# Kernel tuning notes

Hardware: AMD Instinct MI355X
Metric: run time of the kernel (lower is better)

Reference implementation:

```python
import jax, jax.numpy as jnp
import numpy as np

B, N, E, L, S = 8, 64, 256, 128, 2  # graphs, nodes, edges, latent dim, MPN steps


def setup_inputs() -> dict:
    key = jax.random.key(0)
    ks = jax.random.split(key, 16)

    def lin(k, fi, fo):
        return (jax.random.normal(k, (fi, fo), jnp.float32) / np.sqrt(fi).astype(np.float32))

    return {
        "x": jax.random.normal(ks[0], (B, N, L), jnp.float32),
        "edge_attr": jax.random.normal(ks[1], (B, E, L), jnp.float32),
        "u": jax.random.normal(ks[2], (B, L), jnp.float32),
        "spdist": jax.random.uniform(ks[3], (B, N, N), jnp.float32),
        "edge_index": jax.random.randint(ks[4], (B, 2, E), 0, N),
        # encoders
        "W_node_enc": lin(ks[5], 2 * L + 1, L), "b_node_enc": jnp.zeros(L, jnp.float32),
        "W_edge_enc": lin(ks[6], L, L), "b_edge_enc": jnp.zeros(L, jnp.float32),
        "W_glob_enc": lin(ks[7], L, L), "b_glob_enc": jnp.zeros(L, jnp.float32),
        # per-step edge / node update MLPs (stacked over S steps)
        "W_edge_upd": jnp.stack([lin(ks[8 + s], 4 * L, L) for s in range(S)]),
        "b_edge_upd": jnp.zeros((S, L), jnp.float32),
        "W_node_upd": jnp.stack([lin(ks[10 + s], 3 * L, L) for s in range(S)]),
        "b_node_upd": jnp.zeros((S, L), jnp.float32),
        # final edge scorer (per_dest_embedding_to_score)
        "W_score": lin(ks[12], L, 1), "b_score": jnp.zeros(1, jnp.float32),
    }


def reference(x, edge_attr, u, spdist, edge_index,
              W_node_enc, b_node_enc, W_edge_enc, b_edge_enc,
              W_glob_enc, b_glob_enc, W_edge_upd, b_edge_upd,
              W_node_upd, b_node_upd, W_score, b_score):
    act = jax.nn.leaky_relu  # torch LeakyReLU default slope 0.01
    n_steps = W_edge_upd.shape[0]

    def per_graph(xg, eg, ug, sdg, eig):
        Ng, Lg = xg.shape
        Eg = eg.shape[0]
        src, dst = eig[0], eig[1]
        # Augmented node features: graph copy d, node i -> [x_i, x_d, spdist[d, i]]
        # (matches x.repeat(N,1) / x.repeat_interleave(N,0) + chunk(N))
        x_tile = jnp.broadcast_to(xg[None, :, :], (Ng, Ng, Lg))
        x_dest = jnp.broadcast_to(xg[:, None, :], (Ng, Ng, Lg))
        xa = jnp.concatenate([x_tile, x_dest, sdg[..., None]], axis=-1)  # [Nd, N, 2L+1]
        h = act(xa @ W_node_enc + b_node_enc)                            # [Nd, N, L]
        ee = act(eg @ W_edge_enc + b_edge_enc)                           # [E, L]
        ee = jnp.broadcast_to(ee[None], (Ng, Eg, Lg))                    # [Nd, E, L]
        gg = act(ug @ W_glob_enc + b_glob_enc)                           # [L]
        for s in range(n_steps):
            gb_e = jnp.broadcast_to(gg, (Ng, Eg, Lg))
            ein = jnp.concatenate([ee, h[:, src], h[:, dst], gb_e], axis=-1)  # [Nd, E, 4L]
            ee = ee + act(ein @ W_edge_upd[s] + b_edge_upd[s])
            agg = jax.vmap(lambda ef: jax.ops.segment_sum(ef, dst, num_segments=Ng))(ee)  # [Nd, N, L]
            gb_n = jnp.broadcast_to(gg, (Ng, Ng, Lg))
            nin = jnp.concatenate([h, agg, gb_n], axis=-1)                    # [Nd, N, 3L]
            h = h + act(nin @ W_node_upd[s] + b_node_upd[s])
        scores = (ee @ W_score + b_score)[..., 0]  # [Nd, E]
        # reshape(N, -1).t().flatten() per graph -> [E * N]
        return scores.T.reshape(-1)

    out = jax.vmap(per_graph)(x, edge_attr, u, spdist, edge_index)  # [B, E*N]
    return out.reshape(-1)
```

## Files before the change

kernel.cpp:

```cpp
#include <hip/hip_runtime.h>
#include <hip/hip_bf16.h>


typedef __attribute__((ext_vector_type(8))) __bf16 bf16x8;
typedef __attribute__((ext_vector_type(4))) __bf16 bf16x4;
typedef __attribute__((ext_vector_type(4))) float  floatx4;

#define MFMA16(a, b, c) __builtin_amdgcn_mfma_f32_16x16x32_bf16((a), (b), (c), 0, 0, 0)

__device__ __forceinline__ float leaky(float x) { return x > 0.f ? x : 0.01f * x; }

#define WS_WT     0
#define WS_XAP    327680
#define WS_XDP    589824
#define WS_EE0    851968
#define WS_CE     1376256
#define WS_CN     1384448
#define WS_CSROFF 1392640
#define WS_CSREID 1394944

#define LDE 140

__global__ __launch_bounds__(256) void mpn_prep(
    const float* __restrict__ x,
    const float* __restrict__ ea,
    const float* __restrict__ u,
    const int*   __restrict__ eidx,
    const float* __restrict__ Wne,
    const float* __restrict__ bne,
    const float* __restrict__ Wee,
    const float* __restrict__ bee,
    const float* __restrict__ Wge,
    const float* __restrict__ bge,
    const float* __restrict__ Weu,
    const float* __restrict__ beu,
    const float* __restrict__ Wnu,
    const float* __restrict__ bnu,
    char* __restrict__ ws)
{
  __shared__ __align__(16) __bf16 smem[384 * LDE];

  const int b = blockIdx.x, tid = threadIdx.x;
  __bf16* wt  = (__bf16*)(ws + WS_WT);
  float*  xap = (float*)(ws + WS_XAP);
  float*  xdp = (float*)(ws + WS_XDP);
  __bf16* ee0 = (__bf16*)(ws + WS_EE0);
  float*  cev = (float*)(ws + WS_CE);
  float*  cnv = (float*)(ws + WS_CN);
  int* csroff = (int*)(ws + WS_CSROFF);
  int* csreid = (int*)(ws + WS_CSREID);

  if (b < 20) {
    const int m = b >> 1, half = b & 1;
    const int s = m / 5, t = m % 5;
    const float* src = (t < 3) ? (Weu + (size_t)(s*512 + t*128)*128)
                               : (Wnu + (size_t)(s*384 + (t-3)*128)*128);
    for (int it = 0; it < 4; ++it) {
      int p = it*256 + tid;
      int mq = half*4 + (p >> 8);
      int c  = (p >> 6) & 3;
      int l  = p & 63;
      int fr = mq*16 + (l & 15);
      int kb = c*32 + (l >> 4)*8;
      __bf16* dst = &wt[m*16384 + ((mq*4 + c)*64 + l)*8];
      #pragma unroll
      for (int j = 0; j < 8; ++j)
        dst[j] = (__bf16)src[(kb + j)*128 + fr];
    }
  } else if (b < 28) {
    const int g = b - 20;
    __shared__ float gg_sh[128];
    __shared__ int dst_sh[256];
    __shared__ int cnt_sh[64];
    __shared__ int off_sh[65];
    if (tid < 128) {
      float acc = bge[tid];
      for (int k = 0; k < 128; ++k)
        acc += u[g*128 + k] * Wge[k*128 + tid];
      gg_sh[tid] = leaky(acc);
    }
    dst_sh[tid] = eidx[g*512 + 256 + tid];
    __syncthreads();
    {
      const int s = tid >> 7, f = tid & 127;
      float ac = beu[s*128 + f];
      float an = bnu[s*128 + f];
      #pragma unroll 8
      for (int k = 0; k < 128; ++k) {
        float gk = gg_sh[k];
        ac += gk * Weu[(s*512 + 384 + k)*128 + f];
        an += gk * Wnu[(s*384 + 256 + k)*128 + f];
      }
      cev[(g*2 + s)*128 + f] = ac;
      cnv[(g*2 + s)*128 + f] = an;
    }
    if (tid < 64) {
      int c = 0;
      for (int e = 0; e < 256; ++e) c += (dst_sh[e] == tid) ? 1 : 0;
      cnt_sh[tid] = c;
    }
    __syncthreads();
    if (tid == 0) {
      int o = 0;
      for (int n = 0; n < 64; ++n) { off_sh[n] = o; o += cnt_sh[n]; }
      off_sh[64] = o;
    }
    __syncthreads();
    if (tid < 65) csroff[g*72 + tid] = off_sh[tid];
    if (tid < 64) {
      int o = off_sh[tid];
      for (int e = 0; e < 256; ++e)
        if (dst_sh[e] == tid) csreid[g*256 + (o++)] = e;
    }
  } else if (b < 36) {
    const int g = b - 28;
    __bf16* s_a = smem;
    __bf16* s_w = smem + 256*LDE;
    #pragma unroll
    for (int it = 0; it < 32; ++it) {
      int c = it*256 + tid;
      int row = c >> 5, f4 = (c & 31)*4;
      floatx4 v = *(const floatx4*)&ea[(size_t)(g*256 + row)*128 + f4];
      bf16x4 o;
      #pragma unroll
      for (int r = 0; r < 4; ++r) o[r] = (__bf16)v[r];
      *(bf16x4*)&s_a[row*LDE + f4] = o;
    }
    #pragma unroll 8
    for (int it = 0; it < 64; ++it) {
      int k = it*2 + (tid >> 7), f = tid & 127;
      s_w[f*LDE + k] = (__bf16)Wee[k*128 + f];
    }
    __syncthreads();
    const int w = tid >> 6, l = tid & 63, q = l >> 4, xn = l & 15;
    bf16x8 bea[4][4];
    #pragma unroll
    for (int t = 0; t < 4; ++t) {
      int e = w*64 + t*16 + xn;
      #pragma unroll
      for (int c = 0; c < 4; ++c)
        bea[t][c] = *(const bf16x8*)&s_a[e*LDE + c*32 + q*8];
    }
    #pragma unroll
    for (int m = 0; m < 8; ++m) {
      floatx4 acc[4];
      #pragma unroll
      for (int t = 0; t < 4; ++t) acc[t] = (floatx4)0.f;
      const int fr = m*16 + xn;
      #pragma unroll
      for (int c = 0; c < 4; ++c) {
        bf16x8 aw = *(const bf16x8*)&s_w[fr*LDE + c*32 + q*8];
        #pragma unroll
        for (int t = 0; t < 4; ++t) acc[t] = MFMA16(aw, bea[t][c], acc[t]);
      }
      const int f0 = m*16 + q*4;
      floatx4 b4 = *(const floatx4*)&bee[f0];
      #pragma unroll
      for (int t = 0; t < 4; ++t) {
        int e = w*64 + t*16 + xn;
        bf16x4 o;
        #pragma unroll
        for (int r = 0; r < 4; ++r) o[r] = (__bf16)leaky(acc[t][r] + b4[r]);
        *(bf16x4*)&ee0[(size_t)(g*256 + e)*128 + f0] = o;
      }
    }
  } else {
    const int g = b - 36;
    __bf16* s_x  = smem;
    __bf16* s_wa = smem + 64*LDE;
    __bf16* s_wb = smem + 192*LDE;
    #pragma unroll
    for (int it = 0; it < 8; ++it) {
      int c = it*256 + tid;
      int row = c >> 5, f4 = (c & 31)*4;
      floatx4 v = *(const floatx4*)&x[(size_t)(g*64 + row)*128 + f4];
      bf16x4 o;
      #pragma unroll
      for (int r = 0; r < 4; ++r) o[r] = (__bf16)v[r];
      *(bf16x4*)&s_x[row*LDE + f4] = o;
    }
    #pragma unroll 8
    for (int it = 0; it < 64; ++it) {
      int k = it*2 + (tid >> 7), f = tid & 127;
      s_wa[f*LDE + k] = (__bf16)Wne[k*128 + f];
      s_wb[f*LDE + k] = (__bf16)Wne[(128 + k)*128 + f];
    }
    __syncthreads();
    const int w = tid >> 6, l = tid & 63, q = l >> 4, xn = l & 15;
    const int i = w*16 + xn;
    bf16x8 bx[4];
    #pragma unroll
    for (int c = 0; c < 4; ++c)
      bx[c] = *(const bf16x8*)&s_x[i*LDE + c*32 + q*8];
    #pragma unroll
    for (int m = 0; m < 8; ++m) {
      floatx4 aa = (floatx4)0.f, ab = (floatx4)0.f;
      const int fr = m*16 + xn;
      #pragma unroll
      for (int c = 0; c < 4; ++c) {
        bf16x8 aw = *(const bf16x8*)&s_wa[fr*LDE + c*32 + q*8];
        aa = MFMA16(aw, bx[c], aa);
      }
      #pragma unroll
      for (int c = 0; c < 4; ++c) {
        bf16x8 aw = *(const bf16x8*)&s_wb[fr*LDE + c*32 + q*8];
        ab = MFMA16(aw, bx[c], ab);
      }
      const int f0 = m*16 + q*4;
      floatx4 bn4 = *(const floatx4*)&bne[f0];
      floatx4 oa;
      #pragma unroll
      for (int r = 0; r < 4; ++r) oa[r] = aa[r] + bn4[r];
      *(floatx4*)&xap[(size_t)(g*64 + i)*128 + f0] = oa;
      *(floatx4*)&xdp[(size_t)(g*64 + i)*128 + f0] = ab;
    }
  }
}

__global__ __launch_bounds__(512, 2) void mpn_main(
    const float* __restrict__ spdist,
    const int*   __restrict__ eidx,
    const float* __restrict__ Wne,
    const float* __restrict__ wscore,
    const float* __restrict__ bscore,
    const char* __restrict__ ws,
    float* __restrict__ out)
{
  __shared__ __align__(16) __bf16 s_ee[256*LDE];
  __shared__ __align__(16) __bf16 s_h [64*LDE];
  __shared__ __align__(16) __bf16 s_p2[64*LDE];
  __shared__ __align__(16) __bf16 s_p3[64*LDE];
  __shared__ int s_off[65];
  __shared__ int s_eid[256];
  __shared__ float s_sc[256];

  const __bf16* wt  = (const __bf16*)(ws + WS_WT);
  const float*  xap = (const float*)(ws + WS_XAP);
  const float*  xdp = (const float*)(ws + WS_XDP);
  const __bf16* ee0 = (const __bf16*)(ws + WS_EE0);
  const float*  cev = (const float*)(ws + WS_CE);
  const float*  cnv = (const float*)(ws + WS_CN);
  const int* csroff = (const int*)(ws + WS_CSROFF);
  const int* csreid = (const int*)(ws + WS_CSREID);

  const int tid = threadIdx.x;
  const int w = tid >> 6, l = tid & 63;
  const int q = l >> 4, xn = l & 15;
  const int wp = w >> 1, mh = w & 1;
  const int lane8 = l*8;
  const int fme = w*16 + q*4;
  const int g = blockIdx.x >> 6, d = blockIdx.x & 63;

  if (tid < 65) s_off[tid] = csroff[g*72 + tid];
  if (tid < 256) s_eid[tid] = csreid[g*256 + tid];

  {
    const int f = tid & 127, ib = tid >> 7;
    float xdpv = xdp[(g*64 + d)*128 + f];
    float wspv = Wne[256*128 + f];
    #pragma unroll
    for (int j = 0; j < 16; ++j) {
      int i = ib + 4*j;
      float sp = spdist[(g*64 + d)*64 + i];
      float v = xap[(g*64 + i)*128 + f] + xdpv + sp*wspv;
      s_h[i*LDE + f] = (__bf16)leaky(v);
    }
  }
  #pragma unroll
  for (int it = 0; it < 8; ++it) {
    int c = it*512 + tid;
    int row = c >> 4, col = c & 15;
    *(bf16x8*)&s_ee[row*LDE + col*8] = *(const bf16x8*)&ee0[(g*256 + row)*128 + col*8];
  }

  int mySrc[4], myDst[4];
  #pragma unroll
  for (int t = 0; t < 4; ++t) {
    int e = wp*64 + t*16 + xn;
    mySrc[t] = eidx[g*512 + e];
    myDst[t] = eidx[g*512 + 256 + e];
  }
  __syncthreads();

  for (int s = 0; s < 2; ++s) {
    const __bf16* W1T = wt + (s*5 + 0)*16384;
    const __bf16* W2T = wt + (s*5 + 1)*16384;
    const __bf16* W3T = wt + (s*5 + 2)*16384;
    const __bf16* N1T = wt + (s*5 + 3)*16384;
    const __bf16* N2T = wt + (s*5 + 4)*16384;

    bf16x8 w2f[4], w3f[4], n1f[4], n2f[4], w1f[4][4];
    #pragma unroll
    for (int c = 0; c < 4; ++c) {
      w2f[c] = *(const bf16x8*)&W2T[(w*4 + c)*512 + lane8];
      w3f[c] = *(const bf16x8*)&W3T[(w*4 + c)*512 + lane8];
    }
    #pragma unroll
    for (int mm = 0; mm < 4; ++mm)
      #pragma unroll
      for (int c = 0; c < 4; ++c)
        w1f[mm][c] = *(const bf16x8*)&W1T[((mh*4 + mm)*4 + c)*512 + lane8];
    if (s == 0) {
      #pragma unroll
      for (int c = 0; c < 4; ++c) {
        n1f[c] = *(const bf16x8*)&N1T[(w*4 + c)*512 + lane8];
        n2f[c] = *(const bf16x8*)&N2T[(w*4 + c)*512 + lane8];
      }
    }

    {
      floatx4 ce4 = *(const floatx4*)&cev[(g*2 + s)*128 + fme];
      #pragma unroll
      for (int t = 0; t < 4; ++t) {
        const int i = t*16 + xn;
        floatx4 a2 = (floatx4)0.f, a3 = (floatx4)0.f;
        #pragma unroll
        for (int c = 0; c < 4; ++c) {
          bf16x8 bh = *(const bf16x8*)&s_h[i*LDE + c*32 + q*8];
          a2 = MFMA16(w2f[c], bh, a2);
          a3 = MFMA16(w3f[c], bh, a3);
        }
        bf16x4 o2, o3;
        #pragma unroll
        for (int r = 0; r < 4; ++r) { o2[r] = (__bf16)a2[r]; o3[r] = (__bf16)(a3[r] + ce4[r]); }
        *(bf16x4*)&s_p2[i*LDE + fme] = o2;
        *(bf16x4*)&s_p3[i*LDE + fme] = o3;
      }
    }
    floatx4 acc[4][4];
    {
      bf16x8 be[4][4];
      #pragma unroll
      for (int t = 0; t < 4; ++t) {
        int e = wp*64 + t*16 + xn;
        #pragma unroll
        for (int c = 0; c < 4; ++c)
          be[t][c] = *(const bf16x8*)&s_ee[e*LDE + c*32 + q*8];
      }
      #pragma unroll
      for (int mm = 0; mm < 4; ++mm) {
        #pragma unroll
        for (int t = 0; t < 4; ++t) acc[mm][t] = (floatx4)0.f;
        #pragma unroll
        for (int c = 0; c < 4; ++c) {
          #pragma unroll
          for (int t = 0; t < 4; ++t) acc[mm][t] = MFMA16(w1f[mm][c], be[t][c], acc[mm][t]);
        }
      }
    }
    __syncthreads();

    {
      #pragma unroll
      for (int mm = 0; mm < 4; ++mm) {
        const int m = mh*4 + mm;
        const int f0 = m*16 + q*4;
        #pragma unroll
        for (int t = 0; t < 4; ++t) {
          int e = wp*64 + t*16 + xn;
          bf16x4 old = *(const bf16x4*)&s_ee[e*LDE + f0];
          bf16x4 v2  = *(const bf16x4*)&s_p2[mySrc[t]*LDE + f0];
          bf16x4 v3  = *(const bf16x4*)&s_p3[myDst[t]*LDE + f0];
          bf16x4 res;
          #pragma unroll
          for (int r = 0; r < 4; ++r) {
            float vv = acc[mm][t][r] + (float)v2[r] + (float)v3[r];
            res[r] = (__bf16)((float)old[r] + leaky(vv));
          }
          *(bf16x4*)&s_ee[e*LDE + f0] = res;
        }
      }
    }
    __syncthreads();

    if (s == 0) {
      floatx4 a4[4];
      {
        const int node = tid >> 3;
        const int fs = (tid & 7)*16;
        float av[16];
        #pragma unroll
        for (int j = 0; j < 16; ++j) av[j] = 0.f;
        const int b0 = s_off[node], b1 = s_off[node + 1];
        for (int idx = b0; idx < b1; ++idx) {
          int e = s_eid[idx];
          #pragma unroll
          for (int cc = 0; cc < 2; ++cc) {
            bf16x8 vv = *(const bf16x8*)&s_ee[e*LDE + fs + cc*8];
            #pragma unroll
            for (int j = 0; j < 8; ++j) av[cc*8 + j] += (float)vv[j];
          }
        }
        #pragma unroll
        for (int cc = 0; cc < 2; ++cc) {
          bf16x8 o;
          #pragma unroll
          for (int j = 0; j < 8; ++j) o[j] = (__bf16)av[cc*8 + j];
          *(bf16x8*)&s_p2[node*LDE + fs + cc*8] = o;
        }
        #pragma unroll
        for (int t = 0; t < 4; ++t) {
          const int i = t*16 + xn;
          floatx4 a = (floatx4)0.f;
          #pragma unroll
          for (int c = 0; c < 4; ++c) {
            bf16x8 bh = *(const bf16x8*)&s_h[i*LDE + c*32 + q*8];
            a = MFMA16(n1f[c], bh, a);
          }
          a4[t] = a;
        }
      }
      __syncthreads();

      {
        floatx4 cn4 = *(const floatx4*)&cnv[(g*2 + s)*128 + fme];
        #pragma unroll
        for (int t = 0; t < 4; ++t) {
          const int i = t*16 + xn;
          floatx4 a = a4[t];
          #pragma unroll
          for (int c = 0; c < 4; ++c) {
            bf16x8 bg = *(const bf16x8*)&s_p2[i*LDE + c*32 + q*8];
            a = MFMA16(n2f[c], bg, a);
          }
          bf16x4 old = *(const bf16x4*)&s_h[i*LDE + fme];
          bf16x4 res;
          #pragma unroll
          for (int r = 0; r < 4; ++r)
            res[r] = (__bf16)((float)old[r] + leaky(a[r] + cn4[r]));
          *(bf16x4*)&s_h[i*LDE + fme] = res;
        }
      }
      __syncthreads();
    }
  }

  {
    const int e = tid & 255, hh = tid >> 8;
    float acc = 0.f;
    #pragma unroll
    for (int c = 0; c < 8; ++c) {
      bf16x8 vv = *(const bf16x8*)&s_ee[e*LDE + hh*64 + c*8];
      #pragma unroll
      for (int j = 0; j < 8; ++j) acc += (float)vv[j] * wscore[hh*64 + c*8 + j];
    }
    if (hh == 1) s_sc[e] = acc;
    __syncthreads();
    if (hh == 0) out[g*16384 + e*64 + d] = acc + s_sc[e] + bscore[0];
  }
}

extern "C" void kernel_launch(void* const* d_in, const int* in_sizes, int n_in,
                              void* d_out, int out_size, void* d_ws, size_t ws_size,
                              hipStream_t stream) {
  (void)in_sizes; (void)n_in; (void)out_size; (void)ws_size;
  const float* x   = (const float*)d_in[0];
  const float* ea  = (const float*)d_in[1];
  const float* u   = (const float*)d_in[2];
  const float* sp  = (const float*)d_in[3];
  const int*   ei  = (const int*)d_in[4];
  const float* Wne = (const float*)d_in[5];
  const float* bne = (const float*)d_in[6];
  const float* Wee = (const float*)d_in[7];
  const float* bee = (const float*)d_in[8];
  const float* Wge = (const float*)d_in[9];
  const float* bge = (const float*)d_in[10];
  const float* Weu = (const float*)d_in[11];
  const float* beu = (const float*)d_in[12];
  const float* Wnu = (const float*)d_in[13];
  const float* bnu = (const float*)d_in[14];
  const float* Wsc = (const float*)d_in[15];
  const float* bsc = (const float*)d_in[16];
  char* ws = (char*)d_ws;

  hipLaunchKernelGGL(mpn_prep, dim3(44), dim3(256), 0, stream,
                     x, ea, u, ei, Wne, bne, Wee, bee, Wge, bge, Weu, beu, Wnu, bnu, ws);
  hipLaunchKernelGGL(mpn_main, dim3(512), dim3(512), 0, stream,
                     sp, ei, Wne, Wsc, bsc, (const char*)ws, (float*)d_out);
}
```

Baseline: 155.4 us.

## Fuse prep and main kernels into one cooperative launch with grid sync

Merges the preprocessing kernel and the main message-passing kernel into a single cooperative kernel, with a grid-wide sync separating the prep phase from the per-destination computation. The grid shrinks from 512 to 256 blocks, so each block now handles two destination copies in sequence, reloading h and ee each time. This removes one kernel launch and the gap between the two kernels. In exchange it adds a grid barrier, halves the block-level parallelism, and runs the prep phase on only 44 blocks using half their threads.

Result: slower. 323.2 us (+107.9%).

```diff
diff --git a/kernel.cpp b/kernel.cpp
--- a/kernel.cpp
+++ b/kernel.cpp
@@ -1,6 +1,9 @@
 #include <hip/hip_runtime.h>
 #include <hip/hip_bf16.h>
-
+#include <hip/hip_cooperative_groups.h>
+
+
+namespace cg = cooperative_groups;
 
 typedef __attribute__((ext_vector_type(8))) __bf16 bf16x8;
 typedef __attribute__((ext_vector_type(4))) __bf16 bf16x4;
@@ -21,10 +24,11 @@
 
 #define LDE 140
 
-__global__ __launch_bounds__(256) void mpn_prep(
+__global__ __launch_bounds__(512, 2) void mpn_fused(
     const float* __restrict__ x,
     const float* __restrict__ ea,
     const float* __restrict__ u,
+    const float* __restrict__ spdist,
     const int*   __restrict__ eidx,
     const float* __restrict__ Wne,
     const float* __restrict__ bne,
@@ -36,52 +40,67 @@
     const float* __restrict__ beu,
     const float* __restrict__ Wnu,
     const float* __restrict__ bnu,
-    char* __restrict__ ws)
+    const float* __restrict__ wscore,
+    const float* __restrict__ bscore,
+    char* __restrict__ ws,
+    float* __restrict__ out)
 {
-  __shared__ __align__(16) __bf16 smem[384 * LDE];
-
-  const int b = blockIdx.x, tid = threadIdx.x;
-  __bf16* wt  = (__bf16*)(ws + WS_WT);
-  float*  xap = (float*)(ws + WS_XAP);
-  float*  xdp = (float*)(ws + WS_XDP);
-  __bf16* ee0 = (__bf16*)(ws + WS_EE0);
-  float*  cev = (float*)(ws + WS_CE);
-  float*  cnv = (float*)(ws + WS_CN);
-  int* csroff = (int*)(ws + WS_CSROFF);
-  int* csreid = (int*)(ws + WS_CSREID);
-
-  if (b < 20) {
-    const int m = b >> 1, half = b & 1;
-    const int s = m / 5, t = m % 5;
-    const float* src = (t < 3) ? (Weu + (size_t)(s*512 + t*128)*128)
-                               : (Wnu + (size_t)(s*384 + (t-3)*128)*128);
-    for (int it = 0; it < 4; ++it) {
-      int p = it*256 + tid;
-      int mq = half*4 + (p >> 8);
-      int c  = (p >> 6) & 3;
-      int l  = p & 63;
-      int fr = mq*16 + (l & 15);
-      int kb = c*32 + (l >> 4)*8;
-      __bf16* dst = &wt[m*16384 + ((mq*4 + c)*64 + l)*8];
-      #pragma unroll
-      for (int j = 0; j < 8; ++j)
-        dst[j] = (__bf16)src[(kb + j)*128 + fr];
-    }
-  } else if (b < 28) {
-    const int g = b - 20;
-    __shared__ float gg_sh[128];
-    __shared__ int dst_sh[256];
-    __shared__ int cnt_sh[64];
-    __shared__ int off_sh[65];
+  __shared__ __align__(16) __bf16 pool[448 * LDE];
+  __shared__ int s_off[65];
+  __shared__ int s_eid[256];
+  __shared__ float s_sc[256];
+
+  __bf16* s_ee = pool;
+  __bf16* s_h  = pool + 256*LDE;
+  __bf16* s_p2 = pool + 320*LDE;
+  __bf16* s_p3 = pool + 384*LDE;
+
+  __bf16* wt   = (__bf16*)(ws + WS_WT);
+  float*  xap  = (float*)(ws + WS_XAP);
+  float*  xdp  = (float*)(ws + WS_XDP);
+  __bf16* ee0  = (__bf16*)(ws + WS_EE0);
+  float*  cev  = (float*)(ws + WS_CE);
+  float*  cnv  = (float*)(ws + WS_CN);
+  int* csroff  = (int*)(ws + WS_CSROFF);
+  int* csreid  = (int*)(ws + WS_CSREID);
+
+  const int bid = blockIdx.x, tid = threadIdx.x;
+
+  if (bid < 20) {
+    if (tid < 256) {
+      const int m = bid >> 1, half = bid & 1;
+      const int s = m / 5, t = m % 5;
+      const float* src = (t < 3) ? (Weu + (size_t)(s*512 + t*128)*128)
+                                 : (Wnu + (size_t)(s*384 + (t-3)*128)*128);
+      for (int it = 0; it < 4; ++it) {
+        int p = it*256 + tid;
+        int mq = half*4 + (p >> 8);
+        int c  = (p >> 6) & 3;
+        int l  = p & 63;
+        int fr = mq*16 + (l & 15);
+        int kb = c*32 + (l >> 4)*8;
+        __bf16* dst = &wt[m*16384 + ((mq*4 + c)*64 + l)*8];
+        #pragma unroll
+        for (int j = 0; j < 8; ++j)
+          dst[j] = (__bf16)src[(kb + j)*128 + fr];
+      }
+    }
+  } else if (bid < 28) {
+    const int g = bid - 20;
+    char* pb = (char*)pool;
+    float* gg_sh = (float*)pb;
+    int* dst_sh  = (int*)(pb + 512);
+    int* cnt_sh  = (int*)(pb + 1536);
+    int* off_sh  = (int*)(pb + 1792);
     if (tid < 128) {
       float acc = bge[tid];
       for (int k = 0; k < 128; ++k)
         acc += u[g*128 + k] * Wge[k*128 + tid];
       gg_sh[tid] = leaky(acc);
     }
-    dst_sh[tid] = eidx[g*512 + 256 + tid];
-    __syncthreads();
-    {
+    if (tid < 256) dst_sh[tid] = eidx[g*512 + 256 + tid];
+    __syncthreads();
+    if (tid < 256) {
       const int s = tid >> 7, f = tid & 127;
       float ac = beu[s*128 + f];
       float an = bnu[s*128 + f];
@@ -112,166 +131,130 @@
       for (int e = 0; e < 256; ++e)
         if (dst_sh[e] == tid) csreid[g*256 + (o++)] = e;
     }
-  } else if (b < 36) {
-    const int g = b - 28;
-    __bf16* s_a = smem;
-    __bf16* s_w = smem + 256*LDE;
-    #pragma unroll
-    for (int it = 0; it < 32; ++it) {
-      int c = it*256 + tid;
-      int row = c >> 5, f4 = (c & 31)*4;
-      floatx4 v = *(const floatx4*)&ea[(size_t)(g*256 + row)*128 + f4];
-      bf16x4 o;
-      #pragma unroll
-      for (int r = 0; r < 4; ++r) o[r] = (__bf16)v[r];
-      *(bf16x4*)&s_a[row*LDE + f4] = o;
-    }
-    #pragma unroll 8
-    for (int it = 0; it < 64; ++it) {
-      int k = it*2 + (tid >> 7), f = tid & 127;
-      s_w[f*LDE + k] = (__bf16)Wee[k*128 + f];
-    }
-    __syncthreads();
-    const int w = tid >> 6, l = tid & 63, q = l >> 4, xn = l & 15;
-    bf16x8 bea[4][4];
-    #pragma unroll
-    for (int t = 0; t < 4; ++t) {
-      int e = w*64 + t*16 + xn;
-      #pragma unroll
-      for (int c = 0; c < 4; ++c)
-        bea[t][c] = *(const bf16x8*)&s_a[e*LDE + c*32 + q*8];
-    }
-    #pragma unroll
-    for (int m = 0; m < 8; ++m) {
-      floatx4 acc[4];
-      #pragma unroll
-      for (int t = 0; t < 4; ++t) acc[t] = (floatx4)0.f;
-      const int fr = m*16 + xn;
-      #pragma unroll
-      for (int c = 0; c < 4; ++c) {
-        bf16x8 aw = *(const bf16x8*)&s_w[fr*LDE + c*32 + q*8];
-        #pragma unroll
-        for (int t = 0; t < 4; ++t) acc[t] = MFMA16(aw, bea[t][c], acc[t]);
-      }
-      const int f0 = m*16 + q*4;
-      floatx4 b4 = *(const floatx4*)&bee[f0];
+  } else if (bid < 36) {
+    const int g = bid - 28;
+    __bf16* s_a = pool;
+    __bf16* s_w = pool + 256*LDE;
+    if (tid < 256) {
+      #pragma unroll
+      for (int it = 0; it < 32; ++it) {
+        int c = it*256 + tid;
+        int row = c >> 5, f4 = (c & 31)*4;
+        floatx4 v = *(const floatx4*)&ea[(size_t)(g*256 + row)*128 + f4];
+        bf16x4 o;
+        #pragma unroll
+        for (int r = 0; r < 4; ++r) o[r] = (__bf16)v[r];
+        *(bf16x4*)&s_a[row*LDE + f4] = o;
+      }
+      #pragma unroll 8
+      for (int it = 0; it < 64; ++it) {
+        int k = it*2 + (tid >> 7), f = tid & 127;
+        s_w[f*LDE + k] = (__bf16)Wee[k*128 + f];
+      }
+    }
+    __syncthreads();
+    if (tid < 256) {
+      const int w = tid >> 6, l = tid & 63, q = l >> 4, xn = l & 15;
+      bf16x8 bea[4][4];
       #pragma unroll
       for (int t = 0; t < 4; ++t) {
         int e = w*64 + t*16 + xn;
+        #pragma unroll
+        for (int c = 0; c < 4; ++c)
+          bea[t][c] = *(const bf16x8*)&s_a[e*LDE + c*32 + q*8];
+      }
+      #pragma unroll
+      for (int m = 0; m < 8; ++m) {
+        floatx4 acc[4];
+        #pragma unroll
+        for (int t = 0; t < 4; ++t) acc[t] = (floatx4)0.f;
+        const int fr = m*16 + xn;
+        #pragma unroll
+        for (int c = 0; c < 4; ++c) {
+          bf16x8 aw = *(const bf16x8*)&s_w[fr*LDE + c*32 + q*8];
+          #pragma unroll
+          for (int t = 0; t < 4; ++t) acc[t] = MFMA16(aw, bea[t][c], acc[t]);
+        }
+        const int f0 = m*16 + q*4;
+        floatx4 b4 = *(const floatx4*)&bee[f0];
+        #pragma unroll
+        for (int t = 0; t < 4; ++t) {
+          int e = w*64 + t*16 + xn;
+          bf16x4 o;
+          #pragma unroll
+          for (int r = 0; r < 4; ++r) o[r] = (__bf16)leaky(acc[t][r] + b4[r]);
+          *(bf16x4*)&ee0[(size_t)(g*256 + e)*128 + f0] = o;
+        }
+      }
+    }
+  } else if (bid < 44) {
+    const int g = bid - 36;
+    __bf16* s_x  = pool;
+    __bf16* s_wa = pool + 64*LDE;
+    __bf16* s_wb = pool + 192*LDE;
+    if (tid < 256) {
+      #pragma unroll
+      for (int it = 0; it < 8; ++it) {
+        int c = it*256 + tid;
+        int row = c >> 5, f4 = (c & 31)*4;
+        floatx4 v = *(const floatx4*)&x[(size_t)(g*64 + row)*128 + f4];
         bf16x4 o;
         #pragma unroll
-        for (int r = 0; r < 4; ++r) o[r] = (__bf16)leaky(acc[t][r] + b4[r]);
-        *(bf16x4*)&ee0[(size_t)(g*256 + e)*128 + f0] = o;
-      }
-    }
-  } else {
-    const int g = b - 36;
-    __bf16* s_x  = smem;
-    __bf16* s_wa = smem + 64*LDE;
-    __bf16* s_wb = smem + 192*LDE;
-    #pragma unroll
-    for (int it = 0; it < 8; ++it) {
-      int c = it*256 + tid;
-      int row = c >> 5, f4 = (c & 31)*4;
-      floatx4 v = *(const floatx4*)&x[(size_t)(g*64 + row)*128 + f4];
-      bf16x4 o;
-      #pragma unroll
-      for (int r = 0; r < 4; ++r) o[r] = (__bf16)v[r];
-      *(bf16x4*)&s_x[row*LDE + f4] = o;
-    }
-    #pragma unroll 8
-    for (int it = 0; it < 64; ++it) {
-      int k = it*2 + (tid >> 7), f = tid & 127;
-      s_wa[f*LDE + k] = (__bf16)Wne[k*128 + f];
-      s_wb[f*LDE + k] = (__bf16)Wne[(128 + k)*128 + f];
-    }
-    __syncthreads();
-    const int w = tid >> 6, l = tid & 63, q = l >> 4, xn = l & 15;
-    const int i = w*16 + xn;
-    bf16x8 bx[4];
-    #pragma unroll
-    for (int c = 0; c < 4; ++c)
-      bx[c] = *(const bf16x8*)&s_x[i*LDE + c*32 + q*8];
-    #pragma unroll
-    for (int m = 0; m < 8; ++m) {
-      floatx4 aa = (floatx4)0.f, ab = (floatx4)0.f;
-      const int fr = m*16 + xn;
-      #pragma unroll
-      for (int c = 0; c < 4; ++c) {
-        bf16x8 aw = *(const bf16x8*)&s_wa[fr*LDE + c*32 + q*8];
-        aa = MFMA16(aw, bx[c], aa);
-      }
-      #pragma unroll
-      for (int c = 0; c < 4; ++c) {
-        bf16x8 aw = *(const bf16x8*)&s_wb[fr*LDE + c*32 + q*8];
-        ab = MFMA16(aw, bx[c], ab);
-      }
-      const int f0 = m*16 + q*4;
-      floatx4 bn4 = *(const floatx4*)&bne[f0];
-      floatx4 oa;
-      #pragma unroll
-      for (int r = 0; r < 4; ++r) oa[r] = aa[r] + bn4[r];
-      *(floatx4*)&xap[(size_t)(g*64 + i)*128 + f0] = oa;
-      *(floatx4*)&xdp[(size_t)(g*64 + i)*128 + f0] = ab;
+        for (int r = 0; r < 4; ++r) o[r] = (__bf16)v[r];
+        *(bf16x4*)&s_x[row*LDE + f4] = o;
+      }
+      #pragma unroll 8
+      for (int it = 0; it < 64; ++it) {
+        int k = it*2 + (tid >> 7), f = tid & 127;
+        s_wa[f*LDE + k] = (__bf16)Wne[k*128 + f];
+        s_wb[f*LDE + k] = (__bf16)Wne[(128 + k)*128 + f];
+      }
+    }
+    __syncthreads();
+    if (tid < 256) {
+      const int w = tid >> 6, l = tid & 63, q = l >> 4, xn = l & 15;
+      const int i = w*16 + xn;
+      bf16x8 bx[4];
+      #pragma unroll
+      for (int c = 0; c < 4; ++c)
+        bx[c] = *(const bf16x8*)&s_x[i*LDE + c*32 + q*8];
+      #pragma unroll
+      for (int m = 0; m < 8; ++m) {
+        floatx4 aa = (floatx4)0.f, ab = (floatx4)0.f;
+        const int fr = m*16 + xn;
+        #pragma unroll
+        for (int c = 0; c < 4; ++c) {
+          bf16x8 aw = *(const bf16x8*)&s_wa[fr*LDE + c*32 + q*8];
+          aa = MFMA16(aw, bx[c], aa);
+        }
+        #pragma unroll
+        for (int c = 0; c < 4; ++c) {
+          bf16x8 aw = *(const bf16x8*)&s_wb[fr*LDE + c*32 + q*8];
+          ab = MFMA16(aw, bx[c], ab);
+        }
+        const int f0 = m*16 + q*4;
+        floatx4 bn4 = *(const floatx4*)&bne[f0];
+        floatx4 oa;
+        #pragma unroll
+        for (int r = 0; r < 4; ++r) oa[r] = aa[r] + bn4[r];
+        *(floatx4*)&xap[(size_t)(g*64 + i)*128 + f0] = oa;
+        *(floatx4*)&xdp[(size_t)(g*64 + i)*128 + f0] = ab;
+      }
     }
   }
-}
-
-__global__ __launch_bounds__(512, 2) void mpn_main(
-    const float* __restrict__ spdist,
-    const int*   __restrict__ eidx,
-    const float* __restrict__ Wne,
-    const float* __restrict__ wscore,
-    const float* __restrict__ bscore,
-    const char* __restrict__ ws,
-    float* __restrict__ out)
-{
-  __shared__ __align__(16) __bf16 s_ee[256*LDE];
-  __shared__ __align__(16) __bf16 s_h [64*LDE];
-  __shared__ __align__(16) __bf16 s_p2[64*LDE];
-  __shared__ __align__(16) __bf16 s_p3[64*LDE];
-  __shared__ int s_off[65];
-  __shared__ int s_eid[256];
-  __shared__ float s_sc[256];
-
-  const __bf16* wt  = (const __bf16*)(ws + WS_WT);
-  const float*  xap = (const float*)(ws + WS_XAP);
-  const float*  xdp = (const float*)(ws + WS_XDP);
-  const __bf16* ee0 = (const __bf16*)(ws + WS_EE0);
-  const float*  cev = (const float*)(ws + WS_CE);
-  const float*  cnv = (const float*)(ws + WS_CN);
-  const int* csroff = (const int*)(ws + WS_CSROFF);
-  const int* csreid = (const int*)(ws + WS_CSREID);
-
-  const int tid = threadIdx.x;
+
+  __threadfence();
+  cg::this_grid().sync();
+
   const int w = tid >> 6, l = tid & 63;
   const int q = l >> 4, xn = l & 15;
   const int wp = w >> 1, mh = w & 1;
   const int lane8 = l*8;
   const int fme = w*16 + q*4;
-  const int g = blockIdx.x >> 6, d = blockIdx.x & 63;
+  const int g = bid >> 5, dp = bid & 31;
 
   if (tid < 65) s_off[tid] = csroff[g*72 + tid];
   if (tid < 256) s_eid[tid] = csreid[g*256 + tid];
-
-  {
-    const int f = tid & 127, ib = tid >> 7;
-    float xdpv = xdp[(g*64 + d)*128 + f];
-    float wspv = Wne[256*128 + f];
-    #pragma unroll
-    for (int j = 0; j < 16; ++j) {
-      int i = ib + 4*j;
-      float sp = spdist[(g*64 + d)*64 + i];
-      float v = xap[(g*64 + i)*128 + f] + xdpv + sp*wspv;
-      s_h[i*LDE + f] = (__bf16)leaky(v);
-    }
-  }
-  #pragma unroll
-  for (int it = 0; it < 8; ++it) {
-    int c = it*512 + tid;
-    int row = c >> 4, col = c & 15;
-    *(bf16x8*)&s_ee[row*LDE + col*8] = *(const bf16x8*)&ee0[(g*256 + row)*128 + col*8];
-  }
 
   int mySrc[4], myDst[4];
   #pragma unroll
@@ -280,173 +263,196 @@
     mySrc[t] = eidx[g*512 + e];
     myDst[t] = eidx[g*512 + 256 + e];
   }
-  __syncthreads();
-
-  for (int s = 0; s < 2; ++s) {
-    const __bf16* W1T = wt + (s*5 + 0)*16384;
-    const __bf16* W2T = wt + (s*5 + 1)*16384;
-    const __bf16* W3T = wt + (s*5 + 2)*16384;
-    const __bf16* N1T = wt + (s*5 + 3)*16384;
-    const __bf16* N2T = wt + (s*5 + 4)*16384;
-
-    bf16x8 w2f[4], w3f[4], n1f[4], n2f[4], w1f[4][4];
+
+  for (int r = 0; r < 2; ++r) {
+    const int d = dp*2 + r;
+
+    {
+      const int f = tid & 127, ib = tid >> 7;
+      float xdpv = xdp[(g*64 + d)*128 + f];
+      float wspv = Wne[256*128 + f];
+      #pragma unroll
+      for (int j = 0; j < 16; ++j) {
+        int i = ib + 4*j;
+        float sp = spdist[(g*64 + d)*64 + i];
+        float v = xap[(g*64 + i)*128 + f] + xdpv + sp*wspv;
+        s_h[i*LDE + f] = (__bf16)leaky(v);
+      }
+    }
     #pragma unroll
-    for (int c = 0; c < 4; ++c) {
-      w2f[c] = *(const bf16x8*)&W2T[(w*4 + c)*512 + lane8];
-      w3f[c] = *(const bf16x8*)&W3T[(w*4 + c)*512 + lane8];
-    }
-    #pragma unroll
-    for (int mm = 0; mm < 4; ++mm)
-      #pragma unroll
-      for (int c = 0; c < 4; ++c)
-        w1f[mm][c] = *(const bf16x8*)&W1T[((mh*4 + mm)*4 + c)*512 + lane8];
-    if (s == 0) {
+    for (int it = 0; it < 8; ++it) {
+      int c = it*512 + tid;
+      int row = c >> 4, col = c & 15;
+      *(bf16x8*)&s_ee[row*LDE + col*8] = *(const bf16x8*)&ee0[(g*256 + row)*128 + col*8];
+    }
+    __syncthreads();
+
+    for (int s = 0; s < 2; ++s) {
+      const __bf16* W1T = wt + (s*5 + 0)*16384;
+      const __bf16* W2T = wt + (s*5 + 1)*16384;
+      const __bf16* W3T = wt + (s*5 + 2)*16384;
+      const __bf16* N1T = wt + (s*5 + 3)*16384;
+      const __bf16* N2T = wt + (s*5 + 4)*16384;
+
+      bf16x8 w2f[4], w3f[4], n1f[4], n2f[4], w1f[4][4];
       #pragma unroll
       for (int c = 0; c < 4; ++c) {
-        n1f[c] = *(const bf16x8*)&N1T[(w*4 + c)*512 + lane8];
-        n2f[c] = *(const bf16x8*)&N2T[(w*4 + c)*512 + lane8];
-      }
-    }
-
-    {
-      floatx4 ce4 = *(const floatx4*)&cev[(g*2 + s)*128 + fme];
-      #pragma unroll
-      for (int t = 0; t < 4; ++t) {
-        const int i = t*16 + xn;
-        floatx4 a2 = (floatx4)0.f, a3 = (floatx4)0.f;
+        w2f[c] = *(const bf16x8*)&W2T[(w*4 + c)*512 + lane8];
+        w3f[c] = *(const bf16x8*)&W3T[(w*4 + c)*512 + lane8];
+      }
+      #pragma unroll
+      for (int mm = 0; mm < 4; ++mm)
+        #pragma unroll
+        for (int c = 0; c < 4; ++c)
+          w1f[mm][c] = *(const bf16x8*)&W1T[((mh*4 + mm)*4 + c)*512 + lane8];
+      if (s == 0) {
         #pragma unroll
         for (int c = 0; c < 4; ++c) {
-          bf16x8 bh = *(const bf16x8*)&s_h[i*LDE + c*32 + q*8];
-          a2 = MFMA16(w2f[c], bh, a2);
-          a3 = MFMA16(w3f[c], bh, a3);
-        }
-        bf16x4 o2, o3;
-        #pragma unroll
-        for (int r = 0; r < 4; ++r) { o2[r] = (__bf16)a2[r]; o3[r] = (__bf16)(a3[r] + ce4[r]); }
-        *(bf16x4*)&s_p2[i*LDE + fme] = o2;
-        *(bf16x4*)&s_p3[i*LDE + fme] = o3;
-      }
-    }
-    floatx4 acc[4][4];
-    {
-      bf16x8 be[4][4];
-      #pragma unroll
-      for (int t = 0; t < 4; ++t) {
-        int e = wp*64 + t*16 + xn;
-        #pragma unroll
-        for (int c = 0; c < 4; ++c)
-          be[t][c] = *(const bf16x8*)&s_ee[e*LDE + c*32 + q*8];
-      }
-      #pragma unroll
-      for (int mm = 0; mm < 4; ++mm) {
-        #pragma unroll
-        for (int t = 0; t < 4; ++t) acc[mm][t] = (floatx4)0.f;
-        #pragma unroll
-        for (int c = 0; c < 4; ++c) {
-          #pragma unroll
-          for (int t = 0; t < 4; ++t) acc[mm][t] = MFMA16(w1f[mm][c], be[t][c], acc[mm][t]);
-        }
-      }
-    }
-    __syncthreads();
-
-    {
-      #pragma unroll
-      for (int mm = 0; mm < 4; ++mm) {
-        const int m = mh*4 + mm;
-        const int f0 = m*16 + q*4;
+          n1f[c] = *(const bf16x8*)&N1T[(w*4 + c)*512 + lane8];
+          n2f[c] = *(const bf16x8*)&N2T[(w*4 + c)*512 + lane8];
+        }
+      }
+
+      {
+        floatx4 ce4 = *(const floatx4*)&cev[(g*2 + s)*128 + fme];
+        #pragma unroll
+        for (int t = 0; t < 4; ++t) {
+          const int i = t*16 + xn;
+          floatx4 a2 = (floatx4)0.f, a3 = (floatx4)0.f;
+          #pragma unroll
+          for (int c = 0; c < 4; ++c) {
+            bf16x8 bh = *(const bf16x8*)&s_h[i*LDE + c*32 + q*8];
+            a2 = MFMA16(w2f[c], bh, a2);
+            a3 = MFMA16(w3f[c], bh, a3);
+          }
+          bf16x4 o2, o3;
+          #pragma unroll
+          for (int r2 = 0; r2 < 4; ++r2) { o2[r2] = (__bf16)a2[r2]; o3[r2] = (__bf16)(a3[r2] + ce4[r2]); }
+          *(bf16x4*)&s_p2[i*LDE + fme] = o2;
+          *(bf16x4*)&s_p3[i*LDE + fme] = o3;
+        }
+      }
+      floatx4 acc[4][4];
+      {
+        bf16x8 be[4][4];
         #pragma unroll
         for (int t = 0; t < 4; ++t) {
           int e = wp*64 + t*16 + xn;
-          bf16x4 old = *(const bf16x4*)&s_ee[e*LDE + f0];
-          bf16x4 v2  = *(const bf16x4*)&s_p2[mySrc[t]*LDE + f0];
-          bf16x4 v3  = *(const bf16x4*)&s_p3[myDst[t]*LDE + f0];
-          bf16x4 res;
-          #pragma unroll
-          for (int r = 0; r < 4; ++r) {
-            float vv = acc[mm][t][r] + (float)v2[r] + (float)v3[r];
-            res[r] = (__bf16)((float)old[r] + leaky(vv));
-          }
-          *(bf16x4*)&s_ee[e*LDE + f0] = res;
-        }
-      }
-    }
-    __syncthreads();
-
-    if (s == 0) {
-      floatx4 a4[4];
+          #pragma unroll
+          for (int c = 0; c < 4; ++c)
+            be[t][c] = *(const bf16x8*)&s_ee[e*LDE + c*32 + q*8];
+        }
+        #pragma unroll
+        for (int mm = 0; mm < 4; ++mm) {
+          #pragma unroll
+          for (int t = 0; t < 4; ++t) acc[mm][t] = (floatx4)0.f;
+          #pragma unroll
+          for (int c = 0; c < 4; ++c) {
+            #pragma unroll
+            for (int t = 0; t < 4; ++t) acc[mm][t] = MFMA16(w1f[mm][c], be[t][c], acc[mm][t]);
+          }
+        }
+      }
+      __syncthreads();
+
       {
-        const int node = tid >> 3;
-        const int fs = (tid & 7)*16;
-        float av[16];
-        #pragma unroll
-        for (int j = 0; j < 16; ++j) av[j] = 0.f;
-        const int b0 = s_off[node], b1 = s_off[node + 1];
-        for (int idx = b0; idx < b1; ++idx) {
-          int e = s_eid[idx];
+        #pragma unroll
+        for (int mm = 0; mm < 4; ++mm) {
+          const int m = mh*4 + mm;
+          const int f0 = m*16 + q*4;
+          #pragma unroll
+          for (int t = 0; t < 4; ++t) {
+            int e = wp*64 + t*16 + xn;
+            bf16x4 old = *(const bf16x4*)&s_ee[e*LDE + f0];
+            bf16x4 v2  = *(const bf16x4*)&s_p2[mySrc[t]*LDE + f0];
+            bf16x4 v3  = *(const bf16x4*)&s_p3[myDst[t]*LDE + f0];
+            bf16x4 res;
+            #pragma unroll
+            for (int r2 = 0; r2 < 4; ++r2) {
+              float vv = acc[mm][t][r2] + (float)v2[r2] + (float)v3[r2];
+              res[r2] = (__bf16)((float)old[r2] + leaky(vv));
+            }
+            *(bf16x4*)&s_ee[e*LDE + f0] = res;
+          }
+        }
+      }
+      __syncthreads();
+
+      if (s == 0) {
+        floatx4 a4[4];
+        {
+          const int node = tid >> 3;
+          const int fs = (tid & 7)*16;
+          float av[16];
+          #pragma unroll
+          for (int j = 0; j < 16; ++j) av[j] = 0.f;
+          const int b0 = s_off[node], b1 = s_off[node + 1];
+          for (int idx = b0; idx < b1; ++idx) {
+            int e = s_eid[idx];
+            #pragma unroll
+            for (int cc = 0; cc < 2; ++cc) {
+              bf16x8 vv = *(const bf16x8*)&s_ee[e*LDE + fs + cc*8];
+              #pragma unroll
+              for (int j = 0; j < 8; ++j) av[cc*8 + j] += (float)vv[j];
+            }
+          }
           #pragma unroll
           for (int cc = 0; cc < 2; ++cc) {
-            bf16x8 vv = *(const bf16x8*)&s_ee[e*LDE + fs + cc*8];
-            #pragma unroll
-            for (int j = 0; j < 8; ++j) av[cc*8 + j] += (float)vv[j];
-          }
-        }
-        #pragma unroll
-        for (int cc = 0; cc < 2; ++cc) {
-          bf16x8 o;
-          #pragma unroll
-          for (int j = 0; j < 8; ++j) o[j] = (__bf16)av[cc*8 + j];
-          *(bf16x8*)&s_p2[node*LDE + fs + cc*8] = o;
-        }
-        #pragma unroll
-        for (int t = 0; t < 4; ++t) {
-          const int i = t*16 + xn;
-          floatx4 a = (floatx4)0.f;
-          #pragma unroll
-          for (int c = 0; c < 4; ++c) {
-            bf16x8 bh = *(const bf16x8*)&s_h[i*LDE + c*32 + q*8];
-            a = MFMA16(n1f[c], bh, a);
-          }
-          a4[t] = a;
-        }
-      }
+            bf16x8 o;
+            #pragma unroll
+            for (int j = 0; j < 8; ++j) o[j] = (__bf16)av[cc*8 + j];
+            *(bf16x8*)&s_p2[node*LDE + fs + cc*8] = o;
+          }
+          #pragma unroll
+          for (int t = 0; t < 4; ++t) {
+            const int i = t*16 + xn;
+            floatx4 a = (floatx4)0.f;
+            #pragma unroll
+            for (int c = 0; c < 4; ++c) {
+              bf16x8 bh = *(const bf16x8*)&s_h[i*LDE + c*32 + q*8];
+              a = MFMA16(n1f[c], bh, a);
+            }
+            a4[t] = a;
+          }
+        }
+        __syncthreads();
+
+        {
+          floatx4 cn4 = *(const floatx4*)&cnv[(g*2 + s)*128 + fme];
+          #pragma unroll
+          for (int t = 0; t < 4; ++t) {
+            const int i = t*16 + xn;
+            floatx4 a = a4[t];
+            #pragma unroll
+            for (int c = 0; c < 4; ++c) {
+              bf16x8 bg = *(const bf16x8*)&s_p2[i*LDE + c*32 + q*8];
+              a = MFMA16(n2f[c], bg, a);
+            }
+            bf16x4 old = *(const bf16x4*)&s_h[i*LDE + fme];
+            bf16x4 res;
+            #pragma unroll
+            for (int r2 = 0; r2 < 4; ++r2)
+              res[r2] = (__bf16)((float)old[r2] + leaky(a[r2] + cn4[r2]));
+            *(bf16x4*)&s_h[i*LDE + fme] = res;
+          }
+        }
+        __syncthreads();
+      }
+    }
+
+    {
+      const int e = tid & 255, hh = tid >> 8;
+      float acc2 = 0.f;
+      #pragma unroll
+      for (int c = 0; c < 8; ++c) {
+        bf16x8 vv = *(const bf16x8*)&s_ee[e*LDE + hh*64 + c*8];
+        #pragma unroll
+        for (int j = 0; j < 8; ++j) acc2 += (float)vv[j] * wscore[hh*64 + c*8 + j];
+      }
+      if (hh == 1) s_sc[e] = acc2;
       __syncthreads();
-
-      {
-        floatx4 cn4 = *(const floatx4*)&cnv[(g*2 + s)*128 + fme];
-        #pragma unroll
-        for (int t = 0; t < 4; ++t) {
-          const int i = t*16 + xn;
-          floatx4 a = a4[t];
-          #pragma unroll
-          for (int c = 0; c < 4; ++c) {
-            bf16x8 bg = *(const bf16x8*)&s_p2[i*LDE + c*32 + q*8];
-            a = MFMA16(n2f[c], bg, a);
-          }
-          bf16x4 old = *(const bf16x4*)&s_h[i*LDE + fme];
-          bf16x4 res;
-          #pragma unroll
-          for (int r = 0; r < 4; ++r)
-            res[r] = (__bf16)((float)old[r] + leaky(a[r] + cn4[r]));
-          *(bf16x4*)&s_h[i*LDE + fme] = res;
-        }
-      }
-      __syncthreads();
-    }
-  }
-
-  {
-    const int e = tid & 255, hh = tid >> 8;
-    float acc = 0.f;
-    #pragma unroll
-    for (int c = 0; c < 8; ++c) {
-      bf16x8 vv = *(const bf16x8*)&s_ee[e*LDE + hh*64 + c*8];
-      #pragma unroll
-      for (int j = 0; j < 8; ++j) acc += (float)vv[j] * wscore[hh*64 + c*8 + j];
-    }
-    if (hh == 1) s_sc[e] = acc;
-    __syncthreads();
-    if (hh == 0) out[g*16384 + e*64 + d] = acc + s_sc[e] + bscore[0];
+      if (hh == 0) out[g*16384 + e*64 + d] = acc2 + s_sc[e] + bscore[0];
+    }
   }
 }
 
@@ -472,9 +478,10 @@
   const float* Wsc = (const float*)d_in[15];
   const float* bsc = (const float*)d_in[16];
   char* ws = (char*)d_ws;
-
-  hipLaunchKernelGGL(mpn_prep, dim3(44), dim3(256), 0, stream,
-                     x, ea, u, ei, Wne, bne, Wee, bee, Wge, bge, Weu, beu, Wnu, bnu, ws);
-  hipLaunchKernelGGL(mpn_main, dim3(512), dim3(512), 0, stream,
-                     sp, ei, Wne, Wsc, bsc, (const char*)ws, (float*)d_out);
+  float* outp = (float*)d_out;
+
+  void* args[] = { &x, &ea, &u, &sp, &ei, &Wne, &bne, &Wee, &bee, &Wge, &bge,
+                   &Weu, &beu, &Wnu, &bnu, &Wsc, &bsc, &ws, &outp };
+  hipLaunchCooperativeKernel(reinterpret_cast<void*>(mpn_fused),
+                             dim3(256), dim3(512), args, 0, stream);
 }
```
